# Kernel optimization log

Hardware: AMD Instinct MI355X
Metric: run time of the kernel (lower is better)

## Reference

```python
import jax, jax.numpy as jnp
import numpy as np


def setup_inputs() -> dict:
    key = jax.random.key(0)
    ks = jax.random.split(key, 9)
    B, C, H, W = 2, 16, 256, 256
    Cctx = 64
    Cqk, Cv = C // 8, C // 16
    return {
        "x": jax.random.normal(ks[0], (B, C, H, W), jnp.float32),
        "y": jax.random.normal(ks[1], (B, Cctx, H, W), jnp.float32),
        "Wq": jax.random.normal(ks[2], (Cqk, C), jnp.float32) * 0.1,
        "bq": jax.random.normal(ks[3], (Cqk,), jnp.float32) * 0.1,
        "Wk": jax.random.normal(ks[4], (Cqk, C), jnp.float32) * 0.1,
        "bk": jax.random.normal(ks[5], (Cqk,), jnp.float32) * 0.1,
        "Wv": jax.random.normal(ks[6], (Cv, Cctx), jnp.float32) * 0.1,
        "bv": jax.random.normal(ks[7], (Cv,), jnp.float32) * 0.1,
        "gamma": jax.random.normal(ks[8], (1,), jnp.float32),
    }


def reference(x, y, Wq, bq, Wk, bk, Wv, bv, gamma):
    B, C, H, W = x.shape
    # 1x1 convs as channel contractions
    q = jnp.einsum('bchw,oc->bohw', x, Wq) + bq[None, :, None, None]
    k = jnp.einsum('bchw,oc->bohw', x, Wk) + bk[None, :, None, None]
    v = jnp.einsum('bchw,oc->bohw', y, Wv) + bv[None, :, None, None]
    # column (H-axis) attention energy with -inf diagonal: [B,H,W,H]
    eH = jnp.einsum('bchw,bcgw->bhwg', q, k)
    diag = jnp.eye(H, dtype=bool)[None, :, None, :]  # mask h == h2
    eH = jnp.where(diag, -jnp.inf, eH)
    # row (W-axis) attention energy: [B,H,W,W]
    eW = jnp.einsum('bchw,bchg->bhwg', q, k)
    # joint softmax over concatenated H+W axis
    att = jax.nn.softmax(jnp.concatenate([eH, eW], axis=3), axis=3)
    aH, aW = att[..., :H], att[..., H:]
    outH = jnp.einsum('bcgw,bhwg->bchw', v, aH)
    outW = jnp.einsum('bchg,bhwg->bchw', v, aW)
    # bilinear interpolate to (H,W) is an identity here; broadcast Cv=1 over C
    return gamma[0] * (outH + outW) + x
```

## Files before the change

kernel.cpp:

```cpp
#include <hip/hip_runtime.h>
#include <math.h>

#define Bsz  2
#define Cch  16
#define Hdim 256
#define Wdim 256
#define HW   (Hdim * Wdim)
#define BHW  (Bsz * HW)
#define CctxN 64
#define NS   8
#define SG   (Hdim / NS)
#define TH   4
#define LOG2E 1.44269504088896340736f

__device__ __forceinline__ float fexp2(float x) { return exp2f(x); }

__global__ __launch_bounds__(256) void qkv_kernel(
    const float* __restrict__ x, const float* __restrict__ y,
    const float* __restrict__ Wq, const float* __restrict__ bq,
    const float* __restrict__ Wk, const float* __restrict__ bk,
    const float* __restrict__ Wv, const float* __restrict__ bv,
    float2* __restrict__ qpk, float2* __restrict__ kpk, float* __restrict__ v) {
  int idx = blockIdx.x * blockDim.x + threadIdx.x;
  int b  = idx >> 16;
  int hw = idx & (HW - 1);
  const float* xp = x + (size_t)b * Cch * HW + hw;
  float q0 = bq[0], q1 = bq[1], k0 = bk[0], k1 = bk[1];
#pragma unroll
  for (int c = 0; c < Cch; c++) {
    float xv = xp[c * HW];
    q0 = fmaf(Wq[c],       xv, q0);
    q1 = fmaf(Wq[Cch + c], xv, q1);
    k0 = fmaf(Wk[c],       xv, k0);
    k1 = fmaf(Wk[Cch + c], xv, k1);
  }
  qpk[idx] = make_float2(q0 * LOG2E, q1 * LOG2E);
  kpk[idx] = make_float2(k0, k1);
  const float* yp = y + (size_t)b * CctxN * HW + hw;
  float vv = bv[0];
#pragma unroll
  for (int c = 0; c < CctxN; c++) vv = fmaf(Wv[c], yp[c * HW], vv);
  v[idx] = vv;
}

__global__ __launch_bounds__(256, 4) void attn_kernel(
    const float2* __restrict__ qpk, const float2* __restrict__ kpk,
    const float* __restrict__ v, float* __restrict__ part) {
  int s  = blockIdx.x & (NS - 1);
  int ht = (blockIdx.x >> 3) & 63;
  int b  = blockIdx.x >> 9;
  int w  = threadIdx.x;
  int h0 = ht * TH;
  int g0 = s * SG;
  size_t bbase = (size_t)b * HW;

  __shared__ float4 rowpk[TH][SG];
  if (threadIdx.x < TH * SG) {
    int h_l = threadIdx.x >> 5, gg = threadIdx.x & 31;
    size_t ridx = bbase + (size_t)(h0 + h_l) * Wdim + g0 + gg;
    float2 kk = kpk[ridx];
    rowpk[h_l][gg] = make_float4(kk.x, kk.y, v[ridx], 0.f);
  }
  float q0[TH], q1[TH];
#pragma unroll
  for (int h_l = 0; h_l < TH; h_l++) {
    float2 qq = qpk[bbase + (size_t)(h0 + h_l) * Wdim + w];
    q0[h_l] = qq.x; q1[h_l] = qq.y;
  }
  __syncthreads();

  float Z[TH] = {0,0,0,0}, nH[TH] = {0,0,0,0}, nW[TH] = {0,0,0,0};
#pragma unroll 4
  for (int gg = 0; gg < SG; gg++) {
    int g = g0 + gg;
    float2 kc = kpk[bbase + (size_t)g * Wdim + w];
    float  vc = v  [bbase + (size_t)g * Wdim + w];
#pragma unroll
    for (int h_l = 0; h_l < TH; h_l++) {
      float4 r = rowpk[h_l][gg];
      float eH = fmaf(q0[h_l], kc.x, q1[h_l] * kc.y);
      float eW = fmaf(q0[h_l], r.x,  q1[h_l] * r.y);
      float pH = (g == h0 + h_l) ? 0.f : fexp2(eH);
      float pW = fexp2(eW);
      Z [h_l] += pH + pW;
      nH[h_l] = fmaf(pH, vc,  nH[h_l]);
      nW[h_l] = fmaf(pW, r.z, nW[h_l]);
    }
  }
#pragma unroll
  for (int h_l = 0; h_l < TH; h_l++) {
    size_t idx = bbase + (size_t)(h0 + h_l) * Wdim + w;
    part[(size_t)(s * 3 + 0) * BHW + idx] = Z [h_l];
    part[(size_t)(s * 3 + 1) * BHW + idx] = nH[h_l];
    part[(size_t)(s * 3 + 2) * BHW + idx] = nW[h_l];
  }
}

__global__ __launch_bounds__(256) void epi_kernel(
    const float* __restrict__ x, const float* __restrict__ part,
    const float* __restrict__ gamma, float* __restrict__ out) {
  int idx = blockIdx.x * blockDim.x + threadIdx.x;
  float Z = 0.f, nH = 0.f, nW = 0.f;
#pragma unroll
  for (int s2 = 0; s2 < NS; s2++) {
    Z  += part[(size_t)(s2 * 3 + 0) * BHW + idx];
    nH += part[(size_t)(s2 * 3 + 1) * BHW + idx];
    nW += part[(size_t)(s2 * 3 + 2) * BHW + idx];
  }
  float sv = gamma[0] * (nH + nW) / Z;
  int b = idx >> 16, hw = idx & (HW - 1);
  size_t base = (size_t)b * Cch * HW + hw;
#pragma unroll
  for (int c = 0; c < Cch; c++) out[base + c * HW] = sv + x[base + c * HW];
}

extern "C" void kernel_launch(void* const* d_in, const int* in_sizes, int n_in,
                              void* d_out, int out_size, void* d_ws, size_t ws_size,
                              hipStream_t stream) {
  const float* x     = (const float*)d_in[0];
  const float* y     = (const float*)d_in[1];
  const float* Wq    = (const float*)d_in[2];
  const float* bq    = (const float*)d_in[3];
  const float* Wk    = (const float*)d_in[4];
  const float* bk    = (const float*)d_in[5];
  const float* Wv    = (const float*)d_in[6];
  const float* bv    = (const float*)d_in[7];
  const float* gamma = (const float*)d_in[8];
  float* out = (float*)d_out;

  float* ws = (float*)d_ws;
  float2* qpk = (float2*)ws;
  float2* kpk = (float2*)(ws + 2 * BHW);
  float*  v   = ws + 4 * BHW;
  float*  part = ws + 5 * BHW;

  qkv_kernel<<<BHW / 256, 256, 0, stream>>>(x, y, Wq, bq, Wk, bk, Wv, bv, qpk, kpk, v);
  attn_kernel<<<Bsz * (Hdim / TH) * NS, 256, 0, stream>>>(qpk, kpk, v, part);
  epi_kernel<<<BHW / 256, 256, 0, stream>>>(x, part, gamma, out);
}
```

Baseline: 142.4 us.

## Pack k and v into float4, halve split count, vectorize qkv and epilogue

Interleaves k0, k1 and v into a single float4 buffer so the attention inner loop makes one 16-byte load per column instead of two separate loads. The split count over the reduction axis drops from eight to four, which halves the partial-sum traffic and epilogue reads but also halves the grid size. The per-iteration diagonal select is replaced by a subtraction of the diagonal term after the loop, applied only in the split that contains it. The qkv and epilogue kernels now process two pixels per thread with float2 loads and stores, and the occupancy hint on the attention kernel is dropped.

```diff
diff --git a/kernel.cpp b/kernel.cpp
--- a/kernel.cpp
+++ b/kernel.cpp
@@ -8,7 +8,7 @@
 #define HW   (Hdim * Wdim)
 #define BHW  (Bsz * HW)
 #define CctxN 64
-#define NS   8
+#define NS   4
 #define SG   (Hdim / NS)
 #define TH   4
 #define LOG2E 1.44269504088896340736f
@@ -20,46 +20,50 @@
     const float* __restrict__ Wq, const float* __restrict__ bq,
     const float* __restrict__ Wk, const float* __restrict__ bk,
     const float* __restrict__ Wv, const float* __restrict__ bv,
-    float2* __restrict__ qpk, float2* __restrict__ kpk, float* __restrict__ v) {
-  int idx = blockIdx.x * blockDim.x + threadIdx.x;
-  int b  = idx >> 16;
-  int hw = idx & (HW - 1);
-  const float* xp = x + (size_t)b * Cch * HW + hw;
-  float q0 = bq[0], q1 = bq[1], k0 = bk[0], k1 = bk[1];
+    float2* __restrict__ qpk, float4* __restrict__ kv) {
+  int idx0 = (blockIdx.x * blockDim.x + threadIdx.x) * 2;
+  int b  = idx0 >> 16;
+  int hw = idx0 & (HW - 1);
+  const float2* xp = (const float2*)(x + (size_t)b * Cch * HW + hw);
+  float q0a = bq[0], q1a = bq[1], k0a = bk[0], k1a = bk[1];
+  float q0b = bq[0], q1b = bq[1], k0b = bk[0], k1b = bk[1];
 #pragma unroll
   for (int c = 0; c < Cch; c++) {
-    float xv = xp[c * HW];
-    q0 = fmaf(Wq[c],       xv, q0);
-    q1 = fmaf(Wq[Cch + c], xv, q1);
-    k0 = fmaf(Wk[c],       xv, k0);
-    k1 = fmaf(Wk[Cch + c], xv, k1);
+    float2 xv = xp[c * (HW / 2)];
+    q0a = fmaf(Wq[c],       xv.x, q0a);  q0b = fmaf(Wq[c],       xv.y, q0b);
+    q1a = fmaf(Wq[Cch + c], xv.x, q1a);  q1b = fmaf(Wq[Cch + c], xv.y, q1b);
+    k0a = fmaf(Wk[c],       xv.x, k0a);  k0b = fmaf(Wk[c],       xv.y, k0b);
+    k1a = fmaf(Wk[Cch + c], xv.x, k1a);  k1b = fmaf(Wk[Cch + c], xv.y, k1b);
   }
-  qpk[idx] = make_float2(q0 * LOG2E, q1 * LOG2E);
-  kpk[idx] = make_float2(k0, k1);
-  const float* yp = y + (size_t)b * CctxN * HW + hw;
-  float vv = bv[0];
+  qpk[idx0]     = make_float2(q0a * LOG2E, q1a * LOG2E);
+  qpk[idx0 + 1] = make_float2(q0b * LOG2E, q1b * LOG2E);
+  const float2* yp = (const float2*)(y + (size_t)b * CctxN * HW + hw);
+  float va = bv[0], vb2 = bv[0];
 #pragma unroll
-  for (int c = 0; c < CctxN; c++) vv = fmaf(Wv[c], yp[c * HW], vv);
-  v[idx] = vv;
+  for (int c = 0; c < CctxN; c++) {
+    float2 yv = yp[c * (HW / 2)];
+    va  = fmaf(Wv[c], yv.x, va);
+    vb2 = fmaf(Wv[c], yv.y, vb2);
+  }
+  kv[idx0]     = make_float4(k0a, k1a, va,  0.f);
+  kv[idx0 + 1] = make_float4(k0b, k1b, vb2, 0.f);
 }
 
-__global__ __launch_bounds__(256, 4) void attn_kernel(
-    const float2* __restrict__ qpk, const float2* __restrict__ kpk,
-    const float* __restrict__ v, float* __restrict__ part) {
+__global__ __launch_bounds__(256) void attn_kernel(
+    const float2* __restrict__ qpk, const float4* __restrict__ kv,
+    float* __restrict__ part) {
   int s  = blockIdx.x & (NS - 1);
-  int ht = (blockIdx.x >> 3) & 63;
-  int b  = blockIdx.x >> 9;
+  int ht = (blockIdx.x >> 2) & 63;
+  int b  = blockIdx.x >> 8;
   int w  = threadIdx.x;
   int h0 = ht * TH;
   int g0 = s * SG;
   size_t bbase = (size_t)b * HW;
 
-  __shared__ float4 rowpk[TH][SG];
-  if (threadIdx.x < TH * SG) {
-    int h_l = threadIdx.x >> 5, gg = threadIdx.x & 31;
-    size_t ridx = bbase + (size_t)(h0 + h_l) * Wdim + g0 + gg;
-    float2 kk = kpk[ridx];
-    rowpk[h_l][gg] = make_float4(kk.x, kk.y, v[ridx], 0.f);
+  __shared__ float4 rowkv[TH][SG];
+  {
+    int h_l = threadIdx.x >> 6, gg = threadIdx.x & 63;
+    rowkv[h_l][gg] = kv[bbase + (size_t)(h0 + h_l) * Wdim + g0 + gg];
   }
   float q0[TH], q1[TH];
 #pragma unroll
@@ -72,19 +76,24 @@
   float Z[TH] = {0,0,0,0}, nH[TH] = {0,0,0,0}, nW[TH] = {0,0,0,0};
 #pragma unroll 4
   for (int gg = 0; gg < SG; gg++) {
-    int g = g0 + gg;
-    float2 kc = kpk[bbase + (size_t)g * Wdim + w];
-    float  vc = v  [bbase + (size_t)g * Wdim + w];
+    float4 kc = kv[bbase + (size_t)(g0 + gg) * Wdim + w];
 #pragma unroll
     for (int h_l = 0; h_l < TH; h_l++) {
-      float4 r = rowpk[h_l][gg];
-      float eH = fmaf(q0[h_l], kc.x, q1[h_l] * kc.y);
-      float eW = fmaf(q0[h_l], r.x,  q1[h_l] * r.y);
-      float pH = (g == h0 + h_l) ? 0.f : fexp2(eH);
-      float pW = fexp2(eW);
+      float4 r = rowkv[h_l][gg];
+      float pH = fexp2(fmaf(q0[h_l], kc.x, q1[h_l] * kc.y));
+      float pW = fexp2(fmaf(q0[h_l], r.x,  q1[h_l] * r.y));
       Z [h_l] += pH + pW;
-      nH[h_l] = fmaf(pH, vc,  nH[h_l]);
-      nW[h_l] = fmaf(pW, r.z, nW[h_l]);
+      nH[h_l] = fmaf(pH, kc.z, nH[h_l]);
+      nW[h_l] = fmaf(pW, r.z,  nW[h_l]);
+    }
+  }
+  if ((h0 >> 6) == s) {
+#pragma unroll
+    for (int h_l = 0; h_l < TH; h_l++) {
+      float4 kd = kv[bbase + (size_t)(h0 + h_l) * Wdim + w];
+      float pd = fexp2(fmaf(q0[h_l], kd.x, q1[h_l] * kd.y));
+      Z [h_l] -= pd;
+      nH[h_l] = fmaf(-pd, kd.z, nH[h_l]);
     }
   }
 #pragma unroll
@@ -99,19 +108,26 @@
 __global__ __launch_bounds__(256) void epi_kernel(
     const float* __restrict__ x, const float* __restrict__ part,
     const float* __restrict__ gamma, float* __restrict__ out) {
-  int idx = blockIdx.x * blockDim.x + threadIdx.x;
-  float Z = 0.f, nH = 0.f, nW = 0.f;
+  int idx0 = (blockIdx.x * blockDim.x + threadIdx.x) * 2;
+  float2 Z = make_float2(0.f, 0.f), nH = Z, nW = Z;
 #pragma unroll
   for (int s2 = 0; s2 < NS; s2++) {
-    Z  += part[(size_t)(s2 * 3 + 0) * BHW + idx];
-    nH += part[(size_t)(s2 * 3 + 1) * BHW + idx];
-    nW += part[(size_t)(s2 * 3 + 2) * BHW + idx];
+    float2 a = *(const float2*)&part[(size_t)(s2 * 3 + 0) * BHW + idx0];
+    float2 c = *(const float2*)&part[(size_t)(s2 * 3 + 1) * BHW + idx0];
+    float2 d = *(const float2*)&part[(size_t)(s2 * 3 + 2) * BHW + idx0];
+    Z.x += a.x;  Z.y += a.y;
+    nH.x += c.x; nH.y += c.y;
+    nW.x += d.x; nW.y += d.y;
   }
-  float sv = gamma[0] * (nH + nW) / Z;
-  int b = idx >> 16, hw = idx & (HW - 1);
+  float g = gamma[0];
+  float2 sv = make_float2(g * (nH.x + nW.x) / Z.x, g * (nH.y + nW.y) / Z.y);
+  int b = idx0 >> 16, hw = idx0 & (HW - 1);
   size_t base = (size_t)b * Cch * HW + hw;
 #pragma unroll
-  for (int c = 0; c < Cch; c++) out[base + c * HW] = sv + x[base + c * HW];
+  for (int c = 0; c < Cch; c++) {
+    float2 xv = *(const float2*)&x[base + c * HW];
+    *(float2*)&out[base + c * HW] = make_float2(sv.x + xv.x, sv.y + xv.y);
+  }
 }
 
 extern "C" void kernel_launch(void* const* d_in, const int* in_sizes, int n_in,
@@ -130,11 +146,10 @@
 
   float* ws = (float*)d_ws;
   float2* qpk = (float2*)ws;
-  float2* kpk = (float2*)(ws + 2 * BHW);
-  float*  v   = ws + 4 * BHW;
-  float*  part = ws + 5 * BHW;
+  float4* kv  = (float4*)(ws + 2 * BHW);
+  float*  part = ws + 6 * BHW;
 
-  qkv_kernel<<<BHW / 256, 256, 0, stream>>>(x, y, Wq, bq, Wk, bk, Wv, bv, qpk, kpk, v);
-  attn_kernel<<<Bsz * (Hdim / TH) * NS, 256, 0, stream>>>(qpk, kpk, v, part);
-  epi_kernel<<<BHW / 256, 256, 0, stream>>>(x, part, gamma, out);
+  qkv_kernel<<<BHW / 512, 256, 0, stream>>>(x, y, Wq, bq, Wk, bk, Wv, bv, qpk, kv);
+  attn_kernel<<<Bsz * (Hdim / TH) * NS, 256, 0, stream>>>(qpk, kv, part);
+  epi_kernel<<<BHW / 512, 256, 0, stream>>>(x, part, gamma, out);
 }
```

Measured after the change: 129.4 us. -9.1%, faster.
